# Kernel optimization log

Measured on AMD Instinct MI355X. Metric: run time of the kernel, lower is better.

The kernel has to match this reference:

```python
import jax, jax.numpy as jnp
import numpy as np

N, S, E, A = 8192, 128, 128, 8  # num_nodes, state_dim, embed_dim, action_dim


def setup_inputs() -> dict:
    key = jax.random.key(0)
    ks = jax.random.split(key, 12)
    sc = lambda d: 1.0 / np.sqrt(d)  # kaiming-ish fan-in scale
    return {
        "state_matrix": jax.random.normal(ks[0], (N, S), dtype=jnp.float32),
        "adj": jax.random.randint(ks[1], (N, N), 0, 2, dtype=jnp.int32),
        # state_mlp: Linear(S,E) -> ReLU -> Linear(E,E)
        "w1": jax.random.normal(ks[2], (S, E), dtype=jnp.float32) * sc(S),
        "b1": jnp.zeros((E,), dtype=jnp.float32),
        "w2": jax.random.normal(ks[3], (E, E), dtype=jnp.float32) * sc(E),
        "b2": jnp.zeros((E,), dtype=jnp.float32),
        # attention projections (no bias)
        "wq": jax.random.normal(ks[4], (E, E), dtype=jnp.float32) * sc(E),
        "wk": jax.random.normal(ks[5], (E, E), dtype=jnp.float32) * sc(E),
        # head: Linear(E,E) -> ReLU -> Linear(E,A)
        "wh1": jax.random.normal(ks[6], (E, E), dtype=jnp.float32) * sc(E),
        "bh1": jnp.zeros((E,), dtype=jnp.float32),
        "wh2": jax.random.normal(ks[7], (E, A), dtype=jnp.float32) * sc(E),
        "bh2": jnp.zeros((A,), dtype=jnp.float32),
    }


def reference(state_matrix, adj, w1, b1, w2, b2, wq, wk, wh1, bh1, wh2, bh2):
    # state_mlp
    h = jnp.maximum(state_matrix @ w1 + b1, 0.0) @ w2 + b2      # [N, E]
    # scaled dot-product attention masked by adjacency
    q = h @ wq                                                   # [N, E]
    k = h @ wk                                                   # [N, E]
    scores = (q @ k.T) * (1.0 / np.sqrt(E))                      # [N, N]
    scores = jnp.where(adj == 0, -jnp.inf, scores)
    attn = jax.nn.softmax(scores, axis=1)                        # [N, N]
    agg = attn @ h                                               # [N, E]
    # output head
    out = jnp.maximum(agg @ wh1 + bh1, 0.0) @ wh2 + bh2          # [N, A]
    return out
```

## Files before the change

### kernel.cpp

```cpp
#include <hip/hip_runtime.h>
#include <hip/hip_bf16.h>
#include <cstdint>

#define NN 8192
#define EE 128
#define AA 8
#define QSCALE 0.08838834764831845f
#define NKVS 8
#define KVLEN (NN / NKVS)
#define NIT (KVLEN / 64)
#define NW (NN / 64)
#define QTILE 256

typedef __attribute__((ext_vector_type(8))) short bf16x8;
typedef __attribute__((ext_vector_type(16))) float f32x16;
typedef unsigned short u16;
typedef unsigned int u32;
typedef unsigned long long u64;

__device__ __forceinline__ u16 bf16_bits(float x) {
    union { float f; u32 u; } v; v.f = x;
    u32 r = v.u + 0x7fffu + ((v.u >> 16) & 1u);
    return (u16)(r >> 16);
}

__device__ __forceinline__ u32 cvtpk_bf16(float lo, float hi) {
    u32 r;
    asm("v_cvt_pk_bf16_f32 %0, %1, %2" : "=v"(r) : "v"(lo), "v"(hi));
    return r;
}

__global__ __launch_bounds__(256) void k_adjmask(
    const int* __restrict__ adj, u64* __restrict__ msk)
{
    const u32 gwave  = (blockIdx.x * 256 + threadIdx.x) >> 6;
    const u32 nwaves = (gridDim.x * 256) >> 6;
    const int lane   = threadIdx.x & 63;
    const size_t nwords = (size_t)NN * NW;
    for (size_t w = (size_t)gwave * 4; w < nwords; w += (size_t)nwaves * 4) {
        u64 b[4];
        #pragma unroll
        for (int u = 0; u < 4; ++u)
            b[u] = __ballot(adj[(w + u) * 64 + lane] != 0);
        if (lane == 0) {
            *reinterpret_cast<ulonglong2*>(&msk[w])     = ulonglong2{b[0], b[1]};
            *reinterpret_cast<ulonglong2*>(&msk[w + 2]) = ulonglong2{b[2], b[3]};
        }
    }
}

__global__ __launch_bounds__(128) void k_mlp(
    const float* __restrict__ state,
    const float* __restrict__ w1, const float* __restrict__ b1,
    const float* __restrict__ w2, const float* __restrict__ b2,
    const float* __restrict__ wq, const float* __restrict__ wk,
    u16* __restrict__ qb, u16* __restrict__ kb, u16* __restrict__ hT)
{
    __shared__ float st[16][EE + 1];
    __shared__ float h1[16][EE + 1];
    const int t  = threadIdx.x;
    const int ec = (t & 15) * 8;
    const int ra = (t >> 4) * 2, rb = ra + 1;
    const int r0b = blockIdx.x * 16;

    #pragma unroll
    for (int r = 0; r < 16; ++r)
        st[r][t] = state[(size_t)(r0b + r) * EE + t];
    __syncthreads();

    {
        float a0[8], a1[8];
        #pragma unroll
        for (int j = 0; j < 8; ++j) { float b = b1[ec + j]; a0[j] = b; a1[j] = b; }
        for (int s = 0; s < EE; ++s) {
            float x0 = st[ra][s], x1 = st[rb][s];
            const float* wrow = w1 + s * EE + ec;
            #pragma unroll
            for (int j = 0; j < 8; ++j) { float w = wrow[j]; a0[j] = fmaf(x0, w, a0[j]); a1[j] = fmaf(x1, w, a1[j]); }
        }
        __syncthreads();
        #pragma unroll
        for (int j = 0; j < 8; ++j) { h1[ra][ec + j] = fmaxf(a0[j], 0.f); h1[rb][ec + j] = fmaxf(a1[j], 0.f); }
    }
    __syncthreads();

    float hva[8], hvb[8];
    {
        float a0[8], a1[8];
        #pragma unroll
        for (int j = 0; j < 8; ++j) { float b = b2[ec + j]; a0[j] = b; a1[j] = b; }
        for (int s = 0; s < EE; ++s) {
            float x0 = h1[ra][s], x1 = h1[rb][s];
            const float* wrow = w2 + s * EE + ec;
            #pragma unroll
            for (int j = 0; j < 8; ++j) { float w = wrow[j]; a0[j] = fmaf(x0, w, a0[j]); a1[j] = fmaf(x1, w, a1[j]); }
        }
        #pragma unroll
        for (int j = 0; j < 8; ++j) {
            st[ra][ec + j] = a0[j]; st[rb][ec + j] = a1[j];
            hva[j] = a0[j]; hvb[j] = a1[j];
        }
    }
    __syncthreads();

    {
        float q0[8], q1[8], k0[8], k1[8];
        #pragma unroll
        for (int j = 0; j < 8; ++j) { q0[j] = 0.f; q1[j] = 0.f; k0[j] = 0.f; k1[j] = 0.f; }
        for (int s = 0; s < EE; ++s) {
            float x0 = st[ra][s], x1 = st[rb][s];
            const float* wqr = wq + s * EE + ec;
            const float* wkr = wk + s * EE + ec;
            #pragma unroll
            for (int j = 0; j < 8; ++j) {
                float a = wqr[j], b = wkr[j];
                q0[j] = fmaf(x0, a, q0[j]); q1[j] = fmaf(x1, a, q1[j]);
                k0[j] = fmaf(x0, b, k0[j]); k1[j] = fmaf(x1, b, k1[j]);
            }
        }
        bf16x8 vq0, vq1, vk0, vk1;
        #pragma unroll
        for (int j = 0; j < 8; ++j) {
            vq0[j] = (short)bf16_bits(q0[j] * QSCALE);
            vq1[j] = (short)bf16_bits(q1[j] * QSCALE);
            vk0[j] = (short)bf16_bits(k0[j]);
            vk1[j] = (short)bf16_bits(k1[j]);
        }
        *reinterpret_cast<bf16x8*>(qb + (size_t)(r0b + ra) * EE + ec) = vq0;
        *reinterpret_cast<bf16x8*>(qb + (size_t)(r0b + rb) * EE + ec) = vq1;
        *reinterpret_cast<bf16x8*>(kb + (size_t)(r0b + ra) * EE + ec) = vk0;
        *reinterpret_cast<bf16x8*>(kb + (size_t)(r0b + rb) * EE + ec) = vk1;
    }

    #pragma unroll
    for (int j = 0; j < 8; ++j) {
        u32 pack = (u32)bf16_bits(hva[j]) | ((u32)bf16_bits(hvb[j]) << 16);
        *reinterpret_cast<u32*>(hT + (size_t)(ec + j) * NN + r0b + ra) = pack;
    }
}

__global__ __launch_bounds__(512, 2) void k_attn(
    const u16* __restrict__ qb, const u16* __restrict__ kb,
    const u16* __restrict__ hT, const u64* __restrict__ msk,
    _Float16* __restrict__ pacc, float* __restrict__ pm, float* __restrict__ pl)
{
    __shared__ char smem[65536];

    const int tid  = threadIdx.x;
    const int wv   = tid >> 6;
    const int lane = tid & 63;
    const int l31  = lane & 31;
    const int hf   = lane >> 5;
    const int qt   = blockIdx.x >> 3;
    const int kvs  = blockIdx.x & 7;
    const int qr0  = qt * QTILE + wv * 32;
    const int kv0  = kvs * KVLEN;

    bf16x8 qf[8];
    #pragma unroll
    for (int s = 0; s < 8; ++s)
        qf[s] = *reinterpret_cast<const bf16x8*>(
            qb + (size_t)(qr0 + l31) * EE + s * 16 + hf * 8);

    f32x16 acc[4];
    #pragma unroll
    for (int et = 0; et < 4; ++et)
        #pragma unroll
        for (int r = 0; r < 16; ++r) acc[et][r] = 0.f;
    float m = -__builtin_inff(), lsum = 0.f;

    const u64* mrow = msk + (size_t)(qr0 + l31) * NW + kvs * NIT;

    const int kr = tid >> 3, kc = (tid & 7) * 16;
    const int hr = tid >> 2, hc = (tid & 3) * 16;
    const int ksw = (kr & 7) << 4, hsw = (hr & 7) << 4;
    bf16x8 kg[2], hg[2];

    auto LOADG = [&](int c0) {
        kg[0] = *reinterpret_cast<const bf16x8*>(kb + (size_t)(c0 + kr) * EE + kc);
        kg[1] = *reinterpret_cast<const bf16x8*>(kb + (size_t)(c0 + kr) * EE + kc + 8);
        hg[0] = *reinterpret_cast<const bf16x8*>(hT + (size_t)hr * NN + c0 + hc);
        hg[1] = *reinterpret_cast<const bf16x8*>(hT + (size_t)hr * NN + c0 + hc + 8);
    };
    auto WLDS = [&](int b) {
        char* kB = smem + b * 16384;
        *reinterpret_cast<bf16x8*>(kB + kr * 256 + ((kc * 2) ^ ksw))      = kg[0];
        *reinterpret_cast<bf16x8*>(kB + kr * 256 + ((kc * 2 + 16) ^ ksw)) = kg[1];
        char* hB = smem + 32768 + b * 16384;
        *reinterpret_cast<bf16x8*>(hB + hr * 128 + ((hc * 2) ^ hsw))      = hg[0];
        *reinterpret_cast<bf16x8*>(hB + hr * 128 + ((hc * 2 + 16) ^ hsw)) = hg[1];
    };

    LOADG(kv0);
    WLDS(0);
    __syncthreads();

    const int rsw = (l31 & 7) << 4;

    for (int cc = 0; cc < NIT; ++cc) {
        if (cc + 1 < NIT) LOADG(kv0 + (cc + 1) * 64);
        const char* kB = smem + (cc & 1) * 16384;
        const char* hB = smem + 32768 + (cc & 1) * 16384;
        const u64 mw = mrow[cc];

        f32x16 sv0, sv1;
        #pragma unroll
        for (int r = 0; r < 16; ++r) { sv0[r] = 0.f; sv1[r] = 0.f; }
        #pragma unroll
        for (int s = 0; s < 8; ++s) {
            bf16x8 a0 = *reinterpret_cast<const bf16x8*>(
                kB + l31 * 256 + ((s * 32 + hf * 16) ^ rsw));
            sv0 = __builtin_amdgcn_mfma_f32_32x32x16_bf16(a0, qf[s], sv0, 0, 0, 0);
            bf16x8 a1 = *reinterpret_cast<const bf16x8*>(
                kB + (32 + l31) * 256 + ((s * 32 + hf * 16) ^ rsw));
            sv1 = __builtin_amdgcn_mfma_f32_32x32x16_bf16(a1, qf[s], sv1, 0, 0, 0);
        }

        float pv[32];
        float rm = -__builtin_inff();
        #pragma unroll
        for (int r = 0; r < 16; ++r) {
            int k0i = (r & 3) + 8 * (r >> 2) + 4 * hf;
            float v0 = ((mw >> k0i) & 1ull) ? sv0[r] : -__builtin_inff();
            float v1 = ((mw >> (k0i + 32)) & 1ull) ? sv1[r] : -__builtin_inff();
            pv[r] = v0; pv[16 + r] = v1;
            rm = fmaxf(rm, fmaxf(v0, v1));
        }
        rm = fmaxf(rm, __shfl_xor(rm, 32));
        const float mn2 = fmaxf(m, rm);
        const float alpha = (mn2 == m) ? 1.f : __expf(m - mn2);
        const bool noresc = __all(mn2 == m);
        m = mn2;

        float rs = 0.f;
        const bool dead = (mn2 == -__builtin_inff());
        #pragma unroll
        for (int i = 0; i < 32; ++i) {
            float p = dead ? 0.f : __expf(pv[i] - mn2);
            pv[i] = p;
            rs += p;
        }
        rs += __shfl_xor(rs, 32);
        lsum = lsum * alpha + rs;

        u32 w[8][2];
        #pragma unroll
        for (int qd = 0; qd < 8; ++qd) {
            int base = 16 * (qd >> 2) + 4 * (qd & 3);
            w[qd][0] = cvtpk_bf16(pv[base], pv[base + 1]);
            w[qd][1] = cvtpk_bf16(pv[base + 2], pv[base + 3]);
        }

        if (!noresc) {
            #pragma unroll
            for (int et = 0; et < 4; ++et)
                #pragma unroll
                for (int r = 0; r < 16; ++r) acc[et][r] *= alpha;
        }

        #pragma unroll
        for (int s = 0; s < 4; ++s) {
            u32 s0 = hf == 0 ? w[2 * s + 1][0] : w[2 * s][0];
            u32 s1 = hf == 0 ? w[2 * s + 1][1] : w[2 * s][1];
            u32 r0 = __shfl_xor(s0, 32);
            u32 r1 = __shfl_xor(s1, 32);
            union { u32 u[4]; bf16x8 v; } b2;
            b2.u[0] = hf == 0 ? w[2 * s][0] : r0;
            b2.u[1] = hf == 0 ? w[2 * s][1] : r1;
            b2.u[2] = hf == 0 ? r0 : w[2 * s + 1][0];
            b2.u[3] = hf == 0 ? r1 : w[2 * s + 1][1];
            #pragma unroll
            for (int et = 0; et < 4; ++et) {
                bf16x8 a2 = *reinterpret_cast<const bf16x8*>(
                    hB + (32 * et + l31) * 128 + ((s * 32 + hf * 16) ^ rsw));
                acc[et] = __builtin_amdgcn_mfma_f32_32x32x16_bf16(a2, b2.v, acc[et], 0, 0, 0);
            }
        }
        if (cc + 1 < NIT) WLDS((cc + 1) & 1);
        __syncthreads();
    }

    const size_t pbase = (size_t)kvs * NN + qr0;
    #pragma unroll
    for (int et = 0; et < 4; ++et)
        #pragma unroll
        for (int r = 0; r < 16; ++r) {
            int e = 32 * et + (r & 3) + 8 * (r >> 2) + 4 * hf;
            pacc[(pbase + l31) * EE + e] = (_Float16)acc[et][r];
        }
    if (hf == 0) {
        pm[pbase + l31] = m;
        pl[pbase + l31] = lsum;
    }
}

__global__ __launch_bounds__(128) void k_head(
    const _Float16* __restrict__ pacc, const float* __restrict__ pm,
    const float* __restrict__ pl,
    const float* __restrict__ wh1, const float* __restrict__ bh1,
    const float* __restrict__ wh2, const float* __restrict__ bh2,
    float* __restrict__ out)
{
    __shared__ float ag[16][EE + 1];
    __shared__ float h2[16][EE + 1];
    __shared__ float eps[16][NKVS];
    const int t  = threadIdx.x;
    const int ec = (t & 15) * 8;
    const int ra = (t >> 4) * 2, rb = ra + 1;
    const int r0b = blockIdx.x * 16;

    if (t < 16) {
        const int row = r0b + t;
        float mp[NKVS], M = -__builtin_inff();
        #pragma unroll
        for (int p = 0; p < NKVS; ++p) { mp[p] = pm[(size_t)p * NN + row]; M = fmaxf(M, mp[p]); }
        float ep[NKVS], L = 0.f;
        #pragma unroll
        for (int p = 0; p < NKVS; ++p) { ep[p] = __expf(mp[p] - M); L += pl[(size_t)p * NN + row] * ep[p]; }
        const float invL = 1.f / L;
        #pragma unroll
        for (int p = 0; p < NKVS; ++p) eps[t][p] = ep[p] * invL;
    }
    __syncthreads();

    #pragma unroll
    for (int r = 0; r < 16; ++r) {
        float s = 0.f;
        #pragma unroll
        for (int p = 0; p < NKVS; ++p)
            s += (float)pacc[((size_t)p * NN + r0b + r) * EE + t] * eps[r][p];
        ag[r][t] = s;
    }
    __syncthreads();

    {
        float a0[8], a1[8];
        #pragma unroll
        for (int j = 0; j < 8; ++j) { float b = bh1[ec + j]; a0[j] = b; a1[j] = b; }
        for (int s = 0; s < EE; ++s) {
            float x0 = ag[ra][s], x1 = ag[rb][s];
            const float* wrow = wh1 + s * EE + ec;
            #pragma unroll
            for (int j = 0; j < 8; ++j) { float w = wrow[j]; a0[j] = fmaf(x0, w, a0[j]); a1[j] = fmaf(x1, w, a1[j]); }
        }
        #pragma unroll
        for (int j = 0; j < 8; ++j) { h2[ra][ec + j] = fmaxf(a0[j], 0.f); h2[rb][ec + j] = fmaxf(a1[j], 0.f); }
    }
    __syncthreads();
    const int r = t >> 3, a = t & 7;
    float o = bh2[a];
    for (int s = 0; s < EE; ++s) o = fmaf(h2[r][s], wh2[s * AA + a], o);
    out[(size_t)(r0b + r) * AA + a] = o;
}

extern "C" void kernel_launch(void* const* d_in, const int* in_sizes, int n_in,
                              void* d_out, int out_size, void* d_ws, size_t ws_size,
                              hipStream_t stream)
{
    (void)in_sizes; (void)n_in; (void)out_size; (void)ws_size;
    const float* state = (const float*)d_in[0];
    const int*   adj   = (const int*)d_in[1];
    const float* w1  = (const float*)d_in[2];
    const float* b1  = (const float*)d_in[3];
    const float* w2  = (const float*)d_in[4];
    const float* b2  = (const float*)d_in[5];
    const float* wq  = (const float*)d_in[6];
    const float* wk  = (const float*)d_in[7];
    const float* wh1 = (const float*)d_in[8];
    const float* bh1 = (const float*)d_in[9];
    const float* wh2 = (const float*)d_in[10];
    const float* bh2 = (const float*)d_in[11];
    float* out = (float*)d_out;

    char* ws = (char*)d_ws;
    const size_t MB = 1024 * 1024;
    u16*      qb   = (u16*)ws;
    u16*      kb   = (u16*)(ws + 2 * MB);
    u16*      hT   = (u16*)(ws + 4 * MB);
    u64*      msk  = (u64*)(ws + 10 * MB);
    _Float16* pacc = (_Float16*)(ws + 18 * MB);
    float*    pm   = (float*)(ws + 34 * MB);
    float*    pl   = (float*)(ws + 34 * MB + 256 * 1024);

    k_mlp    <<<NN / 16, 128, 0, stream>>>(state, w1, b1, w2, b2, wq, wk, qb, kb, hT);
    k_adjmask<<<2048, 256, 0, stream>>>(adj, msk);
    k_attn   <<<(NN / QTILE) * NKVS, 512, 0, stream>>>(qb, kb, hT, msk, pacc, pm, pl);
    k_head   <<<NN / 16, 128, 0, stream>>>(pacc, pm, pl, wh1, bh1, wh2, bh2, out);
}
```

Baseline: 167.6 us.

## Fuse adjacency bitmask packing and MLP into one interleaved kernel

Merges the adjacency-to-bitmask kernel and the state MLP/QK projection kernel into a single launch. Blocks are interleaved (every ninth block runs the MLP, the rest pack the mask), so the memory-bound adj scan can overlap with the compute-bound MLP. This also removes one kernel launch and the boundary between them. The risk is register and LDS pressure from the MLP path limiting occupancy for the mask-packing blocks.

```diff
diff --git a/kernel.cpp b/kernel.cpp
--- a/kernel.cpp
+++ b/kernel.cpp
@@ -30,26 +30,8 @@
     return r;
 }
 
-__global__ __launch_bounds__(256) void k_adjmask(
-    const int* __restrict__ adj, u64* __restrict__ msk)
-{
-    const u32 gwave  = (blockIdx.x * 256 + threadIdx.x) >> 6;
-    const u32 nwaves = (gridDim.x * 256) >> 6;
-    const int lane   = threadIdx.x & 63;
-    const size_t nwords = (size_t)NN * NW;
-    for (size_t w = (size_t)gwave * 4; w < nwords; w += (size_t)nwaves * 4) {
-        u64 b[4];
-        #pragma unroll
-        for (int u = 0; u < 4; ++u)
-            b[u] = __ballot(adj[(w + u) * 64 + lane] != 0);
-        if (lane == 0) {
-            *reinterpret_cast<ulonglong2*>(&msk[w])     = ulonglong2{b[0], b[1]};
-            *reinterpret_cast<ulonglong2*>(&msk[w + 2]) = ulonglong2{b[2], b[3]};
-        }
-    }
-}
-
-__global__ __launch_bounds__(128) void k_mlp(
+__global__ __launch_bounds__(128) void k_pre(
+    const int* __restrict__ adj, u64* __restrict__ msk,
     const float* __restrict__ state,
     const float* __restrict__ w1, const float* __restrict__ b1,
     const float* __restrict__ w2, const float* __restrict__ b2,
@@ -58,10 +40,31 @@
 {
     __shared__ float st[16][EE + 1];
     __shared__ float h1[16][EE + 1];
-    const int t  = threadIdx.x;
-    const int ec = (t & 15) * 8;
-    const int ra = (t >> 4) * 2, rb = ra + 1;
-    const int r0b = blockIdx.x * 16;
+    const int t = threadIdx.x;
+    const u32 b = blockIdx.x;
+
+    if (b % 9u != 8u) {
+        const u32 ab     = b - (b + 1) / 9u;
+        const u32 gwave  = (ab * 128 + t) >> 6;
+        const u32 nwaves = 8192;
+        const int lane   = t & 63;
+        const size_t nwords = (size_t)NN * NW;
+        for (size_t w = (size_t)gwave * 4; w < nwords; w += (size_t)nwaves * 4) {
+            u64 bb[4];
+            #pragma unroll
+            for (int u = 0; u < 4; ++u)
+                bb[u] = __ballot(adj[(w + u) * 64 + lane] != 0);
+            if (lane == 0) {
+                *reinterpret_cast<ulonglong2*>(&msk[w])     = ulonglong2{bb[0], bb[1]};
+                *reinterpret_cast<ulonglong2*>(&msk[w + 2]) = ulonglong2{bb[2], bb[3]};
+            }
+        }
+        return;
+    }
+
+    const int r0b = (int)(b / 9u) * 16;
+    const int ec  = (t & 15) * 8;
+    const int ra  = (t >> 4) * 2, rb = ra + 1;
 
     #pragma unroll
     for (int r = 0; r < 16; ++r)
@@ -71,7 +74,7 @@
     {
         float a0[8], a1[8];
         #pragma unroll
-        for (int j = 0; j < 8; ++j) { float b = b1[ec + j]; a0[j] = b; a1[j] = b; }
+        for (int j = 0; j < 8; ++j) { float bb = b1[ec + j]; a0[j] = bb; a1[j] = bb; }
         for (int s = 0; s < EE; ++s) {
             float x0 = st[ra][s], x1 = st[rb][s];
             const float* wrow = w1 + s * EE + ec;
@@ -88,7 +91,7 @@
     {
         float a0[8], a1[8];
         #pragma unroll
-        for (int j = 0; j < 8; ++j) { float b = b2[ec + j]; a0[j] = b; a1[j] = b; }
+        for (int j = 0; j < 8; ++j) { float bb = b2[ec + j]; a0[j] = bb; a1[j] = bb; }
         for (int s = 0; s < EE; ++s) {
             float x0 = h1[ra][s], x1 = h1[rb][s];
             const float* wrow = w2 + s * EE + ec;
@@ -113,9 +116,9 @@
             const float* wkr = wk + s * EE + ec;
             #pragma unroll
             for (int j = 0; j < 8; ++j) {
-                float a = wqr[j], b = wkr[j];
+                float a = wqr[j], bb = wkr[j];
                 q0[j] = fmaf(x0, a, q0[j]); q1[j] = fmaf(x1, a, q1[j]);
-                k0[j] = fmaf(x0, b, k0[j]); k1[j] = fmaf(x1, b, k1[j]);
+                k0[j] = fmaf(x0, bb, k0[j]); k1[j] = fmaf(x1, bb, k1[j]);
             }
         }
         bf16x8 vq0, vq1, vk0, vk1;
@@ -382,8 +385,8 @@
     float*    pm   = (float*)(ws + 34 * MB);
     float*    pl   = (float*)(ws + 34 * MB + 256 * 1024);
 
-    k_mlp    <<<NN / 16, 128, 0, stream>>>(state, w1, b1, w2, b2, wq, wk, qb, kb, hT);
-    k_adjmask<<<2048, 256, 0, stream>>>(adj, msk);
-    k_attn   <<<(NN / QTILE) * NKVS, 512, 0, stream>>>(qb, kb, hT, msk, pacc, pm, pl);
-    k_head   <<<NN / 16, 128, 0, stream>>>(pacc, pm, pl, wh1, bh1, wh2, bh2, out);
-}
+    k_pre  <<<4608, 128, 0, stream>>>(adj, msk, state, w1, b1, w2, b2, wq, wk,
+                                      qb, kb, hT);
+    k_attn <<<(NN / QTILE) * NKVS, 512, 0, stream>>>(qb, kb, hT, msk, pacc, pm, pl);
+    k_head <<<NN / 16, 128, 0, stream>>>(pacc, pm, pl, wh1, bh1, wh2, bh2, out);
+}
```

Result: slower. 181.0 us (+8.0%).
